# Kernel optimization log

Hardware: AMD Instinct MI355X
Metric: run time of the kernel (lower is better)

## Reference

```python
import jax, jax.numpy as jnp
import numpy as np

N, D, K = 16384, 256, 4096   # tokens, feature dim, codebook_size
GAMMA = 0.99


def setup_inputs() -> dict:
    key = jax.random.key(0)
    k1, k2, k3 = jax.random.split(key, 3)
    features = jax.random.normal(k1, (N, D), dtype=jnp.float32)
    mask = jax.random.uniform(k2, (N,)) < 0.9
    codebook = jax.random.normal(k3, (K, D), dtype=jnp.float32)  # hk RandomNormal init
    count = jnp.zeros((K,), jnp.float32)
    avg = jnp.zeros((K,), jnp.float32)
    return {"features": features, "mask": mask, "codebook": codebook,
            "count": count, "avg": avg}


def reference(features, mask, codebook, count, avg):
    sg = jax.lax.stop_gradient
    prev_codebook = codebook

    # pairwise squared distances [N, K] via ||f||^2 - 2 f.C^T + ||c||^2
    f2 = jnp.sum(features * features, axis=-1)            # [N]
    c2 = jnp.sum(codebook * codebook, axis=-1)            # [K]
    distance = f2[:, None] - 2.0 * (features @ codebook.T) + c2[None, :]
    distance = jnp.where(mask[:, None], distance, jnp.inf)

    assign_fwd = jnp.argmin(distance, axis=1)             # [N] nearest code per token
    assign_rev = jnp.argmin(distance, axis=0)             # [K] nearest token per code
    features_fwd = codebook[assign_fwd]                   # [N, D]
    features_rev = features[assign_rev]                   # [K, D]

    # straight-through estimator
    out_features = sg(features_fwd) + features - sg(features)

    total = jnp.maximum(mask.sum(), 1).astype(features.dtype)
    commitment = jnp.mean((sg(features_fwd) - features) ** 2, axis=-1)
    commitment_loss = jnp.where(mask, commitment, 0.0).sum() / total

    # scatter-add assignment counts (masked) and feature sums (unmasked, as in source)
    assignment_count = jnp.zeros((K,), jnp.float32).at[assign_fwd].add(
        mask.astype(jnp.float32))
    assignment_mask = assignment_count < 1

    count = (1.0 - GAMMA) * assignment_count + GAMMA * count
    avg = (1.0 - GAMMA) * assignment_count / total + GAMMA * avg
    alpha = jnp.exp(-avg * K * 10.0 / (1.0 - GAMMA) - 0.001)

    feat_sum = jnp.zeros_like(codebook).at[assign_fwd].add(features)  # [K, D]
    assigned_update = (GAMMA * codebook + (1.0 - GAMMA) * feat_sum)
    assigned_update = assigned_update / jnp.maximum(count[:, None], 1.0)
    unassigned_update = (1.0 - alpha)[:, None] * codebook + alpha[:, None] * features_rev
    new_codebook = jnp.where(assignment_mask[:, None], assigned_update, unassigned_update)

    # pmean(delta) is identity on a single device; final = prev + (prev - new), as in source
    codebook_delta = prev_codebook - new_codebook
    new_codebook = prev_codebook + codebook_delta

    unassigned_percent = (assignment_count > 0).mean()
    return (out_features, assign_fwd, commitment_loss, unassigned_percent,
            count, avg, new_codebook)
```

## Files before the change

### kernel.cpp

```cpp
#include <hip/hip_runtime.h>
#include <math.h>

typedef unsigned long long u64;
typedef unsigned int u32;

#define N_TOK 16384
#define DIM   256
#define KCB   4096

#define WS_ROWMIN   0
#define WS_COLMIN   131072
#define WS_CNT      163840
#define WS_CPART    180224
#define WS_TOTAL    181248
#define WS_FLAG     181252
#define WS_F2       181312
#define WS_C2       246848
#define WS_END      263232

#define OUT_FEAT    0
#define OUT_ASSIGN  4194304
#define OUT_CLOSS   4210688
#define OUT_UPCT    4210689
#define OUT_COUNT   4210690
#define OUT_AVG     4214786
#define OUT_CB      4218882

#define C_1MG 0.009999999776482582f

__device__ __forceinline__ u32 fkey(float d) {
    u32 u = __float_as_uint(d);
    return (u & 0x80000000u) ? ~u : (u | 0x80000000u);
}
__device__ __forceinline__ u64 u64min(u64 a, u64 b) { return a < b ? a : b; }
__device__ __forceinline__ u64 shflxor64(u64 v, int m) {
    int lo = __shfl_xor((int)(u32)(v & 0xFFFFFFFFULL), m, 64);
    int hi = __shfl_xor((int)(u32)(v >> 32), m, 64);
    return ((u64)(u32)hi << 32) | (u32)lo;
}
__device__ __forceinline__ bool read_mask(const void* mp, int flag, int n) {
    if (flag == 2) return ((const float*)mp)[n] != 0.0f;
    if (flag == 1) return ((const int*)mp)[n] != 0;
    return ((const unsigned char*)mp)[n] != 0;
}
__device__ __forceinline__ void gload_lds16(const void* g, void* l) {
    __builtin_amdgcn_global_load_lds((const __attribute__((address_space(1))) void*)g,
                                     (__attribute__((address_space(3))) void*)l,
                                     16, 0, 0);
}

__global__ void k_detect(const void* __restrict__ mp, int* __restrict__ flag) {
    if (threadIdx.x == 0) {
        const u32* w = (const u32*)mp;
        bool allf = true, alli = true, any1 = false;
        for (int i = 0; i < 64; ++i) {
            u32 x = w[i];
            if (x != 0u && x != 0x3F800000u) allf = false;
            if (x == 0x3F800000u) any1 = true;
            if (x > 1u) alli = false;
        }
        *flag = (allf && any1) ? 2 : (alli ? 1 : 0);
    }
}

__global__ __launch_bounds__(256)
void k_norms(const float* __restrict__ F, const float* __restrict__ CB,
             const void* __restrict__ mp, const int* __restrict__ flagp,
             float* __restrict__ f2, float* __restrict__ c2) {
    __shared__ float red[4];
    const int b = blockIdx.x, d = threadIdx.x;
    const float* src = (b < N_TOK) ? (F + (size_t)b * DIM) : (CB + (size_t)(b - N_TOK) * DIM);
    float v = src[d];
    float s = v * v;
#pragma unroll
    for (int m = 32; m > 0; m >>= 1) s += __shfl_xor(s, m, 64);
    if ((d & 63) == 0) red[d >> 6] = s;
    __syncthreads();
    if (d == 0) {
        float tot = red[0] + red[1] + red[2] + red[3];
        if (b < N_TOK) {
            bool msk = read_mask(mp, *flagp, b);
            f2[b] = msk ? tot : __builtin_huge_valf();
        } else {
            c2[b - N_TOK] = tot;
        }
    }
}

__global__ __launch_bounds__(256)
void k_gemm(const float* __restrict__ F, const float* __restrict__ CB,
            const float* __restrict__ f2, const float* __restrict__ c2,
            u64* __restrict__ rowmin, u64* __restrict__ colmin) {
    __shared__ float As[128 * 32];
    __shared__ float Bs[128 * 32];
    __shared__ u64 colred[4][128];

    const int t = threadIdx.x;
    const int tx = t & 15;
    const int ty = t >> 4;
    const int wave = t >> 6;
    const int rowbase = blockIdx.x * 128;
    const int kbase = blockIdx.y * 128;

    float acc[8][8];
#pragma unroll
    for (int i = 0; i < 8; ++i)
#pragma unroll
        for (int j = 0; j < 8; ++j) acc[i][j] = 0.0f;

    const char* gA[4];
    const char* gB[4];
#pragma unroll
    for (int p = 0; p < 4; ++p) {
        const int idx = p * 256 + t;
        const int r = idx >> 3;
        const int c4 = (idx & 7) << 2;
        const int sc = c4 ^ ((r & 7) << 2);
        gA[p] = (const char*)(F + (size_t)(rowbase + r) * DIM + sc);
        gB[p] = (const char*)(CB + (size_t)(kbase + r) * DIM + sc);
    }
    char* AsB = (char*)As;
    char* BsB = (char*)Bs;
    const int aswz = (ty & 7) << 2;
    const int bswz = (tx & 7) << 2;

    for (int ch = 0; ch < 8; ++ch) {
#pragma unroll
        for (int p = 0; p < 4; ++p) {
            const int ldsb = p * 4096 + wave * 1024;
            gload_lds16(gA[p] + ch * 128, AsB + ldsb);
            gload_lds16(gB[p] + ch * 128, BsB + ldsb);
        }
        __syncthreads();
#pragma unroll
        for (int dd = 0; dd < 32; dd += 4) {
            const int ca = dd ^ aswz, cb = dd ^ bswz;
            float4 a[8], b[8];
#pragma unroll
            for (int i = 0; i < 8; ++i)
                a[i] = *(const float4*)&As[(ty + i * 16) * 32 + ca];
#pragma unroll
            for (int j = 0; j < 8; ++j)
                b[j] = *(const float4*)&Bs[(tx + j * 16) * 32 + cb];
#pragma unroll
            for (int i = 0; i < 8; ++i)
#pragma unroll
                for (int j = 0; j < 8; ++j) {
                    acc[i][j] = fmaf(a[i].x, b[j].x, acc[i][j]);
                    acc[i][j] = fmaf(a[i].y, b[j].y, acc[i][j]);
                    acc[i][j] = fmaf(a[i].z, b[j].z, acc[i][j]);
                    acc[i][j] = fmaf(a[i].w, b[j].w, acc[i][j]);
                }
        }
        __syncthreads();
    }

    float c2k[8];
#pragma unroll
    for (int j = 0; j < 8; ++j) c2k[j] = c2[kbase + tx + j * 16];
    u64 cbst[8];
#pragma unroll
    for (int j = 0; j < 8; ++j) cbst[j] = ~0ULL;

#pragma unroll
    for (int i = 0; i < 8; ++i) {
        const int row = rowbase + ty + i * 16;
        const float f2r = f2[row];
        u64 rbst = ~0ULL;
#pragma unroll
        for (int j = 0; j < 8; ++j) {
            float dist = (f2r - 2.0f * acc[i][j]) + c2k[j];
            u64 hk = (u64)fkey(dist) << 32;
            rbst    = u64min(rbst, hk | (u32)(kbase + tx + j * 16));
            cbst[j] = u64min(cbst[j], hk | (u32)row);
        }
        rbst = u64min(rbst, shflxor64(rbst, 1));
        rbst = u64min(rbst, shflxor64(rbst, 2));
        rbst = u64min(rbst, shflxor64(rbst, 4));
        rbst = u64min(rbst, shflxor64(rbst, 8));
        if (tx == 0) atomicMin(&rowmin[row], rbst);
    }

#pragma unroll
    for (int j = 0; j < 8; ++j) {
        cbst[j] = u64min(cbst[j], shflxor64(cbst[j], 16));
        cbst[j] = u64min(cbst[j], shflxor64(cbst[j], 32));
    }
    if ((t & 63) < 16) {
#pragma unroll
        for (int j = 0; j < 8; ++j) colred[wave][tx + j * 16] = cbst[j];
    }
    __syncthreads();
    if (t < 128) {
        u64 m = u64min(u64min(colred[0][t], colred[1][t]),
                       u64min(colred[2][t], colred[3][t]));
        atomicMin(&colmin[kbase + t], m);
    }
}

__global__ __launch_bounds__(256)
void k_token(const float* __restrict__ F, const float* __restrict__ CB,
             const u64* __restrict__ rowmin, const void* __restrict__ mp,
             const int* __restrict__ flagp,
             float* __restrict__ out_feat, float* __restrict__ out_assign,
             float* __restrict__ cnt, float* __restrict__ fsum,
             float* __restrict__ cpart) {
    __shared__ float red[4];
    const int n = blockIdx.x, d = threadIdx.x;
    const int k = (int)(u32)(rowmin[n] & 0xFFFFFFFFULL);
    const float f = F[(size_t)n * DIM + d];
    const float cv = CB[(size_t)k * DIM + d];
    out_feat[(size_t)n * DIM + d] = (cv + f) - f;
    const float df = cv - f;
    float s = df * df;
#pragma unroll
    for (int m = 32; m > 0; m >>= 1) s += __shfl_xor(s, m, 64);
    if ((d & 63) == 0) red[d >> 6] = s;
    __syncthreads();
    atomicAdd(&fsum[(size_t)k * DIM + d], f);
    if (d == 0) {
        out_assign[n] = (float)k;
        bool msk = read_mask(mp, *flagp, n);
        if (msk) {
            float tot = red[0] + red[1] + red[2] + red[3];
            atomicAdd(&cnt[k], 1.0f);
            atomicAdd(&cpart[n & 255], tot * (1.0f / 256.0f));
        }
    }
}

__global__ __launch_bounds__(256)
void k_scalars(const float* __restrict__ cnt, const float* __restrict__ cpart,
               float* __restrict__ totf, float* __restrict__ out) {
    __shared__ float redf[4], redc[4];
    __shared__ int redi[4];
    const int t = threadIdx.x;
    float ts = 0.0f;
    int asg = 0;
    for (int i = t; i < KCB; i += 256) {
        float v = cnt[i];
        ts += v;
        asg += (v > 0.0f) ? 1 : 0;
    }
    float cs = cpart[t];
#pragma unroll
    for (int m = 32; m > 0; m >>= 1) {
        ts += __shfl_xor(ts, m, 64);
        cs += __shfl_xor(cs, m, 64);
        asg += __shfl_xor(asg, m, 64);
    }
    if ((t & 63) == 0) { redf[t >> 6] = ts; redc[t >> 6] = cs; redi[t >> 6] = asg; }
    __syncthreads();
    if (t == 0) {
        float total = redf[0] + redf[1] + redf[2] + redf[3];
        total = fmaxf(total, 1.0f);
        float closs = (redc[0] + redc[1] + redc[2] + redc[3]) / total;
        int a = redi[0] + redi[1] + redi[2] + redi[3];
        totf[0] = total;
        out[OUT_CLOSS] = closs;
        out[OUT_UPCT] = (float)a / 4096.0f;
    }
}

__global__ __launch_bounds__(256)
void k_cbupd(const float* __restrict__ F, const float* __restrict__ CB,
             const float* __restrict__ cnt_in, const float* __restrict__ avg_in,
             const float* __restrict__ ac_, const float* __restrict__ fsum,
             const u64* __restrict__ colmin, const float* __restrict__ totf,
             float* __restrict__ out_count, float* __restrict__ out_avg,
             float* __restrict__ out_cb) {
    const int k = blockIdx.x, d = threadIdx.x;
    const float ac = ac_[k];
    const float total = totf[0];
    const float cn = C_1MG * ac + 0.99f * cnt_in[k];
    const float av = (C_1MG * ac) / total + 0.99f * avg_in[k];
    const float arg = ((-av * 4096.0f) * 10.0f) / C_1MG - 0.001f;
    const float alpha = expf(arg);
    const int tok = (int)(u32)(colmin[k] & 0xFFFFFFFFULL);
    const float cb = CB[(size_t)k * DIM + d];
    const float fs = fsum[(size_t)k * DIM + d];
    const float fr = F[(size_t)tok * DIM + d];
    const float assigned = (0.99f * cb + C_1MG * fs) / fmaxf(cn, 1.0f);
    const float unass = (1.0f - alpha) * cb + alpha * fr;
    const float nc = (ac < 1.0f) ? assigned : unass;
    out_cb[(size_t)k * DIM + d] = cb + (cb - nc);
    if (d == 0) { out_count[k] = cn; out_avg[k] = av; }
}

extern "C" void kernel_launch(void* const* d_in, const int* in_sizes, int n_in,
                              void* d_out, int out_size, void* d_ws, size_t ws_size,
                              hipStream_t stream) {
    const float* F   = (const float*)d_in[0];
    const void*  Mp  = d_in[1];
    const float* CB  = (const float*)d_in[2];
    const float* CNT = (const float*)d_in[3];
    const float* AVG = (const float*)d_in[4];
    float* out = (float*)d_out;
    char* ws = (char*)d_ws;
    if (ws_size < (size_t)WS_END) return;

    u64*   rowmin = (u64*)(ws + WS_ROWMIN);
    u64*   colmin = (u64*)(ws + WS_COLMIN);
    float* cnt    = (float*)(ws + WS_CNT);
    float* cpart  = (float*)(ws + WS_CPART);
    float* totf   = (float*)(ws + WS_TOTAL);
    int*   flag   = (int*)(ws + WS_FLAG);
    float* f2     = (float*)(ws + WS_F2);
    float* c2     = (float*)(ws + WS_C2);
    float* fsum   = out + OUT_CB;

    hipMemsetAsync(ws, 0xFF, 163840, stream);
    hipMemsetAsync(ws + WS_CNT, 0, WS_FLAG - WS_CNT, stream);
    hipMemsetAsync(fsum, 0, (size_t)KCB * DIM * sizeof(float), stream);

    k_detect<<<1, 64, 0, stream>>>(Mp, flag);
    k_norms<<<N_TOK + KCB, 256, 0, stream>>>(F, CB, Mp, flag, f2, c2);
    k_gemm<<<dim3(128, 32), 256, 0, stream>>>(F, CB, f2, c2, rowmin, colmin);
    k_token<<<N_TOK, 256, 0, stream>>>(F, CB, rowmin, Mp, flag,
                                       out + OUT_FEAT, out + OUT_ASSIGN,
                                       cnt, fsum, cpart);
    k_scalars<<<1, 256, 0, stream>>>(cnt, cpart, totf, out);
    k_cbupd<<<KCB, 256, 0, stream>>>(F, CB, CNT, AVG, cnt, fsum, colmin, totf,
                                     out + OUT_COUNT, out + OUT_AVG, out + OUT_CB);
}
```

Measured before the change: 548.4 us.

## Double-buffer LDS tiles in distance GEMM to overlap global loads with FMA

Doubles the shared-memory A/B tiles and issues direct-to-LDS global loads for chunk ch+1 before computing chunk ch, waiting only on the previous chunk's loads with a partial vmcnt. Barriers become raw s_barrier. The aim is to hide global-load latency behind the FP32 FMA loop. The cost is twice the LDS per block, which may lower occupancy, and the correctness now depends on hand-written waitcnt counts.

New measurement: 699.4 us. 1.28x slower.

```diff
diff --git a/kernel.cpp b/kernel.cpp
--- a/kernel.cpp
+++ b/kernel.cpp
@@ -91,8 +91,8 @@
 void k_gemm(const float* __restrict__ F, const float* __restrict__ CB,
             const float* __restrict__ f2, const float* __restrict__ c2,
             u64* __restrict__ rowmin, u64* __restrict__ colmin) {
-    __shared__ float As[128 * 32];
-    __shared__ float Bs[128 * 32];
+    __shared__ float As[2 * 128 * 32];
+    __shared__ float Bs[2 * 128 * 32];
     __shared__ u64 colred[4][128];
 
     const int t = threadIdx.x;
@@ -124,24 +124,38 @@
     const int aswz = (ty & 7) << 2;
     const int bswz = (tx & 7) << 2;
 
+#define STAGE(ch)                                                         \
+    {                                                                     \
+        const int half_ = ((ch) & 1) ? 16384 : 0;                         \
+        _Pragma("unroll")                                                 \
+        for (int p = 0; p < 4; ++p) {                                     \
+            const int ldsb_ = half_ + p * 4096 + wave * 1024;             \
+            gload_lds16(gA[p] + (ch) * 128, AsB + ldsb_);                 \
+            gload_lds16(gB[p] + (ch) * 128, BsB + ldsb_);                 \
+        }                                                                 \
+    }
+
+    STAGE(0);
     for (int ch = 0; ch < 8; ++ch) {
-#pragma unroll
-        for (int p = 0; p < 4; ++p) {
-            const int ldsb = p * 4096 + wave * 1024;
-            gload_lds16(gA[p] + ch * 128, AsB + ldsb);
-            gload_lds16(gB[p] + ch * 128, BsB + ldsb);
-        }
-        __syncthreads();
+        if (ch < 7) {
+            STAGE(ch + 1);
+            asm volatile("s_waitcnt vmcnt(8)" ::: "memory");
+        } else {
+            asm volatile("s_waitcnt vmcnt(0)" ::: "memory");
+        }
+        __builtin_amdgcn_s_barrier();
+        const float* Ab = As + ((ch & 1) ? 4096 : 0);
+        const float* Bb = Bs + ((ch & 1) ? 4096 : 0);
 #pragma unroll
         for (int dd = 0; dd < 32; dd += 4) {
             const int ca = dd ^ aswz, cb = dd ^ bswz;
             float4 a[8], b[8];
 #pragma unroll
             for (int i = 0; i < 8; ++i)
-                a[i] = *(const float4*)&As[(ty + i * 16) * 32 + ca];
+                a[i] = *(const float4*)&Ab[(ty + i * 16) * 32 + ca];
 #pragma unroll
             for (int j = 0; j < 8; ++j)
-                b[j] = *(const float4*)&Bs[(tx + j * 16) * 32 + cb];
+                b[j] = *(const float4*)&Bb[(tx + j * 16) * 32 + cb];
 #pragma unroll
             for (int i = 0; i < 8; ++i)
 #pragma unroll
@@ -152,7 +166,7 @@
                     acc[i][j] = fmaf(a[i].w, b[j].w, acc[i][j]);
                 }
         }
-        __syncthreads();
+        __builtin_amdgcn_s_barrier();
     }
 
     float c2k[8];
```
